# Optimization experiments

Hardware: AMD Instinct MI355X
Metric: run time of the kernel (lower is better)

Reference implementation:

```python
import jax, jax.numpy as jnp
import numpy as np

EPS_PD = 1e-6    # torch F.pairwise_distance eps (added to x - y before norm)
EPS_NORM = 1e-12  # torch F.normalize eps


def l2_normalize(x):
    n = jnp.sqrt(jnp.sum(x * x, axis=1, keepdims=True))
    return x / jnp.maximum(n, EPS_NORM)


def pairwise_l2(x, y):
    # Faithful to ||x_i - y_j + eps||_2 (torch pairwise_distance adds scalar eps
    # to every coordinate of the difference) but computed via Gram matrices
    D = x.shape[1]
    xx = jnp.sum(x * x, axis=1)            # [B]
    yy = jnp.sum(y * y, axis=1)            # [B]
    xy = x @ y.T                           # [B, B]
    sq = xx[:, None] + yy[None, :] - 2.0 * xy
    # cross terms from the +eps shift: 2*eps*sum(x_i - y_j) + D*eps^2
    sq = sq + 2.0 * EPS_PD * (jnp.sum(x, axis=1)[:, None] - jnp.sum(y, axis=1)[None, :])
    sq = sq + D * (EPS_PD * EPS_PD)
    return jnp.sqrt(jnp.maximum(sq, 0.0))


def setup_inputs() -> dict:
    key = jax.random.key(0)
    k1, k2 = jax.random.split(key)
    B, D = 4096, 512
    low_feature = jax.random.normal(k1, (B, D), dtype=jnp.float32)
    embed_feature = jax.random.normal(k2, (B, D), dtype=jnp.float32)
    id_numpy = jnp.arange(B, dtype=jnp.int64 if jax.config.read('jax_enable_x64') else jnp.int32).reshape(B, 1)
    return {"low_feature": low_feature, "embed_feature": embed_feature, "id_numpy": id_numpy}


def reference(low_feature, embed_feature, id_numpy):
    # ids are unique (arange), so the set()-dedup in the original is identity.
    B = low_feature.shape[0]
    K = B  # k_num == current_batch_size -> x_start = y_start = 0

    low_n = l2_normalize(low_feature)
    emb_n = l2_normalize(embed_feature)

    dist_low = pairwise_l2(low_n, low_n)      # [B, B]
    dist_embed = pairwise_l2(emb_n, emb_n)    # [B, B]

    dl1 = dist_low[: K - 1, : K - 2]
    dl2 = dist_low[: K - 1, 1 : K - 1]
    de1 = dist_embed[: K - 1, : K - 2]
    de2 = dist_embed[: K - 1, 1 : K - 1]

    coeff = jnp.sign(dl1 - dl2) - jnp.sign(de1 - de2)
    dist_embed_inverse = de2 - de1
    loss_structure = jnp.mean(coeff * dist_embed_inverse)
    return loss_structure
```

## Files before the change

### kernel.cpp

```cpp
#include <hip/hip_runtime.h>
#include <hip/hip_bf16.h>
#include <hip/hip_fp8.h>
#include <math.h>

#define BROWS 4096
#define DIM   512
#define YEMB_B 2097152
#define TSTRIDE 191
#define NT 22

typedef float f32x4 __attribute__((ext_vector_type(4)));

__global__ __launch_bounds__(256) void prep4_kernel(
    const float* __restrict__ low, const float* __restrict__ emb,
    unsigned char* __restrict__ Yq,
    float* __restrict__ s_l, float* __restrict__ r_l,
    float* __restrict__ s_e, float* __restrict__ r_e,
    float* __restrict__ out) {
  const int tid = threadIdx.x;
  const int lane = tid & 63, wid = tid >> 6;
  const int rid = blockIdx.x * 4 + wid;
  if (blockIdx.x == 0 && tid == 0) out[0] = 0.f;

  const bool is_low = (rid < BROWS);
  const int row = is_low ? rid : rid - BROWS;
  const float* x = (is_low ? low : emb) + (size_t)row * DIM;

  const float4 v0 = ((const float4*)x)[lane * 2];
  const float4 v1 = ((const float4*)x)[lane * 2 + 1];

  float ss = v0.x * v0.x + v0.y * v0.y + v0.z * v0.z + v0.w * v0.w +
             v1.x * v1.x + v1.y * v1.y + v1.z * v1.z + v1.w * v1.w;
#pragma unroll
  for (int o = 1; o < 64; o <<= 1) ss += __shfl_xor(ss, o, 64);
  const float inv = 1.0f / fmaxf(sqrtf(ss), 1e-12f);

  float y[8] = {v0.x * inv, v0.y * inv, v0.z * inv, v0.w * inv,
                v1.x * inv, v1.y * inv, v1.z * inv, v1.w * inv};

  union { unsigned char b[8]; unsigned long long u; } pk;
  float sv = 0.f, rv = 0.f;
#pragma unroll
  for (int i = 0; i < 8; ++i) {
    pk.b[i] = __hip_fp8_e4m3(y[i]).__x;
    sv += y[i] * y[i];
    rv += y[i];
  }
  ((unsigned long long*)(Yq + (size_t)rid * 512))[lane] = pk.u;

#pragma unroll
  for (int o = 1; o < 64; o <<= 1) {
    sv += __shfl_xor(sv, o, 64);
    rv += __shfl_xor(rv, o, 64);
  }
  if (lane == 0) {
    (is_low ? s_l : s_e)[row] = sv;
    (is_low ? r_l : r_e)[row] = rv;
  }
}

__global__ __launch_bounds__(256, 2) void fused_sym_kernel(
    const unsigned char* __restrict__ Yq,
    const float* __restrict__ s_l, const float* __restrict__ r_l,
    const float* __restrict__ s_e, const float* __restrict__ r_e,
    float* __restrict__ out) {
  __shared__ __align__(16) long lds_l[9728];
  __shared__ __align__(16) float aE[192];
  __shared__ __align__(16) float bE[120];
  __shared__ __align__(16) float cL[120];
  __shared__ float sred[4];

  const int b2 = blockIdx.x >> 1;
  const int half = blockIdx.x & 1;
  const int br = b2 / NT;
  const int bc = b2 % NT;

  const int tid = threadIdx.x;
  const int lane = tid & 63;
  const int wid = tid >> 6;
  const int wr = wid;
  const int quad = lane >> 4, cpos = lane & 15;
  const int r0 = br * TSTRIDE;
  const int cB = bc * TSTRIDE + half * 96;
  const int tcbase = half * 96;
  const float epst = (float)DIM * 1e-6f * 1e-6f;

  if (tid < 192) {
    const int gi = min(r0 + tid, BROWS - 1);
    aE[tid] = s_e[gi] + 2e-6f * r_e[gi] + epst;
  }
  if (tid < 116) {
    const int gj = min(cB + tid, BROWS - 1);
    const int gj1 = min(cB + tid + 1, BROWS - 1);
    bE[tid] = s_e[gj] - 2e-6f * r_e[gj];
    cL[tid] = (s_l[gj] - s_l[gj1]) - 2e-6f * (r_l[gj] - r_l[gj1]);
  }

  int goff[10];
#pragma unroll
  for (int s = 0; s < 10; ++s) {
    const int c = tid + 256 * s;
    const int rp = c >> 3, cc = c & 7;
    int seg, rpl;
    if (rp < 96)       { seg = 0; rpl = rp;       }
    else if (rp < 192) { seg = 1; rpl = rp - 96;  }
    else if (rp < 248) { seg = 2; rpl = rp - 192; }
    else               { seg = 3; rpl = rp - 248; }
    const int rloc = 2 * rpl + (cc >> 2);
    const int gch = (cc & 3) ^ (rpl & 3);
    int base;
    if (seg == 0)      base = min(r0 + rloc, BROWS - 1) * 512;
    else if (seg == 1) base = YEMB_B + min(r0 + rloc, BROWS - 1) * 512;
    else if (seg == 2) base = min(cB + rloc, BROWS - 1) * 512;
    else               base = YEMB_B + min(cB + rloc, BROWS - 1) * 512;
    goff[s] = base + (gch << 4);
  }

  auto STAGE = [&](int t, int b) {
    const int k0 = t * 64;
#pragma unroll
    for (int s = 0; s < 10; ++s) {
      if (s < 9 || tid < 128)
        __builtin_amdgcn_global_load_lds(
            (const __attribute__((address_space(1))) void*)(Yq + goff[s] + k0),
            (__attribute__((address_space(3))) void*)(
                ((char*)lds_l) + b * 38912 + (tid + 256 * s) * 16),
            16, 0, 0);
    }
  };

  const int RaH = (48 * wr + cpos) >> 1;
  const int s3a = RaH & 3;
  const int aoff = RaH * 128 + (cpos & 1) * 64 + (quad & 1) * 8;
  const int s3b = (cpos >> 1) & 3;
  const int boff = (cpos >> 1) * 128 + (cpos & 1) * 64 + (quad & 1) * 8;
  const int iaL = aoff >> 3;
  const int iaE = (12288 + aoff) >> 3;
  const int ibL = (24576 + boff) >> 3;
  const int ibE = (31744 + boff) >> 3;

  f32x4 accl[7][3], acce[7][3];
#pragma unroll
  for (int jb = 0; jb < 7; ++jb)
#pragma unroll
    for (int ib = 0; ib < 3; ++ib) {
      accl[jb][ib] = (f32x4)(0.f);
      acce[jb][ib] = (f32x4)(0.f);
    }

  STAGE(0, 0);

  for (int t = 0; t < 8; ++t) {
    if (t < 7) STAGE(t + 1, (t + 1) & 1);
    if (t == 7)       asm volatile("s_waitcnt vmcnt(0)" ::: "memory");
    else if (wid < 2) asm volatile("s_waitcnt vmcnt(10)" ::: "memory");
    else              asm volatile("s_waitcnt vmcnt(9)" ::: "memory");
    __builtin_amdgcn_s_barrier();
    __builtin_amdgcn_sched_barrier(0);

    const int bo = (t & 1) * 4864;
#pragma unroll
    for (int kk = 0; kk < 2; ++kk) {
      const int q = 2 * kk + (quad >> 1);
      const int qa2 = ((q ^ s3a) << 1);
      const int qb2 = ((q ^ s3b) << 1);
      {
        long a[7], b[3];
#pragma unroll
        for (int jb = 0; jb < 7; ++jb) a[jb] = lds_l[bo + ibL + qb2 + jb * 128];
#pragma unroll
        for (int ib = 0; ib < 3; ++ib) b[ib] = lds_l[bo + iaL + qa2 + ib * 128];
        __builtin_amdgcn_s_setprio(1);
#pragma unroll
        for (int jb = 0; jb < 7; ++jb)
#pragma unroll
          for (int ib = 0; ib < 3; ++ib)
            accl[jb][ib] = __builtin_amdgcn_mfma_f32_16x16x32_fp8_fp8(
                a[jb], b[ib], accl[jb][ib], 0, 0, 0);
        __builtin_amdgcn_s_setprio(0);
      }
      {
        long a[7], b[3];
#pragma unroll
        for (int jb = 0; jb < 7; ++jb) a[jb] = lds_l[bo + ibE + qb2 + jb * 128];
#pragma unroll
        for (int ib = 0; ib < 3; ++ib) b[ib] = lds_l[bo + iaE + qa2 + ib * 128];
        __builtin_amdgcn_s_setprio(1);
#pragma unroll
        for (int jb = 0; jb < 7; ++jb)
#pragma unroll
          for (int ib = 0; ib < 3; ++ib)
            acce[jb][ib] = __builtin_amdgcn_mfma_f32_16x16x32_fp8_fp8(
                a[jb], b[ib], acce[jb][ib], 0, 0, 0);
        __builtin_amdgcn_s_setprio(0);
      }
    }
    __builtin_amdgcn_sched_barrier(0);
    __builtin_amdgcn_s_barrier();
    __builtin_amdgcn_sched_barrier(0);
  }

  float sum = 0.f;

#pragma unroll
  for (int ib = 0; ib < 3; ++ib) {
    const int irow = 48 * wr + 16 * ib + cpos;
    const int gi = r0 + irow;
    const bool rowok = (irow <= TSTRIDE - 1) && (gi <= BROWS - 2);
    const float ai = aE[irow];

    float deJ[4], glJ[4];
    {
      const float4 bj = ((const float4*)bE)[quad];
#pragma unroll
      for (int r = 0; r < 4; ++r) {
        deJ[r] = sqrtf(fmaxf(ai + bj[r] - 2.f * acce[0][ib][r], 0.f));
        glJ[r] = accl[0][ib][r];
      }
    }

#pragma unroll
    for (int jb = 0; jb < 6; ++jb) {
      const float4 bn = ((const float4*)bE)[4 * (jb + 1) + quad];
      float deN[4], glN[4];
#pragma unroll
      for (int r = 0; r < 4; ++r) {
        deN[r] = sqrtf(fmaxf(ai + bn[r] - 2.f * acce[jb + 1][ib][r], 0.f));
        glN[r] = accl[jb + 1][ib][r];
      }
      const float deq = __shfl(deJ[0], (lane + 16) & 63, 64);
      const float dec = __shfl(deN[0], lane & 15, 64);
      const float glq = __shfl(glJ[0], (lane + 16) & 63, 64);
      const float glc = __shfl(glN[0], lane & 15, 64);
      const float de2r3 = (quad < 3) ? deq : dec;
      const float gl2r3 = (quad < 3) ? glq : glc;

      const float4 cl = ((const float4*)cL)[4 * jb + quad];
#pragma unroll
      for (int r = 0; r < 4; ++r) {
        const float de1 = deJ[r];
        const float de2 = (r < 3) ? deJ[r + 1] : de2r3;
        const float g2 = (r < 3) ? glJ[r + 1] : gl2r3;
        const float x = de2 - de1;
        const float Dl = cl[r] - 2.f * (glJ[r] - g2);
        const float tterm = fabsf(x) +
                            (Dl > 0.f ? x : (Dl < 0.f ? -x : 0.f));
        const int jcol = tcbase + 16 * jb + 4 * quad + r;
        const int gj = cB + 16 * jb + 4 * quad + r;
        if (rowok && jcol <= TSTRIDE - 1 && gj <= BROWS - 3) sum += tterm;
      }
#pragma unroll
      for (int r = 0; r < 4; ++r) { deJ[r] = deN[r]; glJ[r] = glN[r]; }
    }
  }

#pragma unroll
  for (int o = 32; o; o >>= 1) sum += __shfl_down(sum, o, 64);
  if (lane == 0) sred[wid] = sum;
  __syncthreads();
  if (tid == 0) {
    const float scale = 1.0f / ((float)(BROWS - 1) * (float)(BROWS - 2));
    float t = 0.f;
#pragma unroll
    for (int w = 0; w < 4; ++w) t += sred[w];
    atomicAdd(out, t * scale);
  }
}

extern "C" void kernel_launch(void* const* d_in, const int* in_sizes, int n_in,
                              void* d_out, int out_size, void* d_ws,
                              size_t ws_size, hipStream_t stream) {
  const float* low = (const float*)d_in[0];
  const float* emb = (const float*)d_in[1];
  float* out = (float*)d_out;

  unsigned char* Yq = (unsigned char*)d_ws;
  float* s_l = (float*)(Yq + 2 * (size_t)BROWS * DIM);
  float* r_l = s_l + BROWS;
  float* s_e = r_l + BROWS;
  float* r_e = s_e + BROWS;

  prep4_kernel<<<2 * BROWS / 4, 256, 0, stream>>>(low, emb, Yq, s_l, r_l, s_e, r_e, out);
  fused_sym_kernel<<<NT * NT * 2, 256, 0, stream>>>(Yq, s_l, r_l, s_e, r_e, out);
}
```

Baseline: 119.8 us.

## Exploit Gram matrix symmetry to compute only upper-triangular tiles

Launches only the upper-triangular tile pairs (br<=bc) and, for off-diagonal tiles, also evaluates the transposed contribution by taking differences along rows instead of columns. Cross-tile neighbors come from shuffles and a small LDS hand-off buffer. This roughly halves the MFMA and load work. The K loop also changes to 32-byte stages with a triple-buffered LDS pipeline and a new swizzle, and the unused seventh column block in the odd half is skipped. It adds extra epilogue shuffles and LDS traffic, and the boundary masking is tricky and could be wrong.

```diff
diff --git a/kernel.cpp b/kernel.cpp
--- a/kernel.cpp
+++ b/kernel.cpp
@@ -64,21 +64,24 @@
     const float* __restrict__ s_l, const float* __restrict__ r_l,
     const float* __restrict__ s_e, const float* __restrict__ r_e,
     float* __restrict__ out) {
-  __shared__ __align__(16) long lds_l[9728];
+  __shared__ __align__(16) long lds_l[7680];
   __shared__ __align__(16) float aE[192];
   __shared__ __align__(16) float bE[120];
   __shared__ __align__(16) float cL[120];
+  __shared__ __align__(16) float cLi[192];
+  __shared__ float hand[3][112][2];
   __shared__ float sred[4];
 
-  const int b2 = blockIdx.x >> 1;
   const int half = blockIdx.x & 1;
-  const int br = b2 / NT;
-  const int bc = b2 % NT;
+  int rem = blockIdx.x >> 1, br = 0;
+  while (rem >= NT - br) { rem -= NT - br; ++br; }
+  const int bc = br + rem;
+  const bool diag = (br == bc);
+  const bool hasv6 = (half == 0);
 
   const int tid = threadIdx.x;
   const int lane = tid & 63;
-  const int wid = tid >> 6;
-  const int wr = wid;
+  const int wr = tid >> 6;
   const int quad = lane >> 4, cpos = lane & 15;
   const int r0 = br * TSTRIDE;
   const int cB = bc * TSTRIDE + half * 96;
@@ -87,7 +90,9 @@
 
   if (tid < 192) {
     const int gi = min(r0 + tid, BROWS - 1);
+    const int gi1 = min(r0 + tid + 1, BROWS - 1);
     aE[tid] = s_e[gi] + 2e-6f * r_e[gi] + epst;
+    cLi[tid] = (s_l[gi] - s_l[gi1]) + 2e-6f * (r_l[gi] - r_l[gi1]);
   }
   if (tid < 116) {
     const int gj = min(cB + tid, BROWS - 1);
@@ -96,48 +101,50 @@
     cL[tid] = (s_l[gj] - s_l[gj1]) - 2e-6f * (r_l[gj] - r_l[gj1]);
   }
 
-  int goff[10];
-#pragma unroll
-  for (int s = 0; s < 10; ++s) {
+  int goff[5];
+#pragma unroll
+  for (int s = 0; s < 5; ++s) {
     const int c = tid + 256 * s;
-    const int rp = c >> 3, cc = c & 7;
-    int seg, rpl;
-    if (rp < 96)       { seg = 0; rpl = rp;       }
-    else if (rp < 192) { seg = 1; rpl = rp - 96;  }
-    else if (rp < 248) { seg = 2; rpl = rp - 192; }
-    else               { seg = 3; rpl = rp - 248; }
-    const int rloc = 2 * rpl + (cc >> 2);
-    const int gch = (cc & 3) ^ (rpl & 3);
-    int base;
-    if (seg == 0)      base = min(r0 + rloc, BROWS - 1) * 512;
-    else if (seg == 1) base = YEMB_B + min(r0 + rloc, BROWS - 1) * 512;
-    else if (seg == 2) base = min(cB + rloc, BROWS - 1) * 512;
-    else               base = YEMB_B + min(cB + rloc, BROWS - 1) * 512;
-    goff[s] = base + (gch << 4);
+    int seg, base;
+    if (c < 384)      { seg = 0; base = 0; }
+    else if (c < 768) { seg = 1; base = 384; }
+    else if (c < 992) { seg = 2; base = 768; }
+    else              { seg = 3; base = 992; }
+    const int within = c - base;
+    const int rpl = within >> 2, cc = within & 3;
+    const int rloc = 2 * rpl + ((cc >> 1) ^ ((rpl >> 1) & 1));
+    const int g = (cc & 1) ^ (rpl & 1);
+    int rowb;
+    if (seg == 0)      rowb = min(r0 + rloc, BROWS - 1) * 512;
+    else if (seg == 1) rowb = YEMB_B + min(r0 + rloc, BROWS - 1) * 512;
+    else if (seg == 2) rowb = min(cB + rloc, BROWS - 1) * 512;
+    else               rowb = YEMB_B + min(cB + rloc, BROWS - 1) * 512;
+    goff[s] = rowb + g * 16;
   }
 
   auto STAGE = [&](int t, int b) {
-    const int k0 = t * 64;
-#pragma unroll
-    for (int s = 0; s < 10; ++s) {
-      if (s < 9 || tid < 128)
+    const int k0 = t * 32;
+#pragma unroll
+    for (int s = 0; s < 5; ++s) {
+      if (s < 4 || tid < 192)
         __builtin_amdgcn_global_load_lds(
             (const __attribute__((address_space(1))) void*)(Yq + goff[s] + k0),
             (__attribute__((address_space(3))) void*)(
-                ((char*)lds_l) + b * 38912 + (tid + 256 * s) * 16),
+                ((char*)lds_l) + b * 20480 + (tid + 256 * s) * 16),
             16, 0, 0);
     }
   };
 
   const int RaH = (48 * wr + cpos) >> 1;
-  const int s3a = RaH & 3;
-  const int aoff = RaH * 128 + (cpos & 1) * 64 + (quad & 1) * 8;
-  const int s3b = (cpos >> 1) & 3;
-  const int boff = (cpos >> 1) * 128 + (cpos & 1) * 64 + (quad & 1) * 8;
-  const int iaL = aoff >> 3;
-  const int iaE = (12288 + aoff) >> 3;
-  const int ibL = (24576 + boff) >> 3;
-  const int ibE = (31744 + boff) >> 3;
+  const int offA = RaH * 64 + (((cpos & 1) ^ ((RaH >> 1) & 1)) << 5) +
+                   (((quad >> 1) ^ (RaH & 1)) << 4) + (quad & 1) * 8;
+  const int RbH = cpos >> 1;
+  const int offB = RbH * 64 + (((cpos & 1) ^ ((RbH >> 1) & 1)) << 5) +
+                   (((quad >> 1) ^ (RbH & 1)) << 4) + (quad & 1) * 8;
+  const int iaL = offA >> 3;
+  const int iaE = (6144 + offA) >> 3;
+  const int ibL = (12288 + offB) >> 3;
+  const int ibE = (15872 + offB) >> 3;
 
   f32x4 accl[7][3], acce[7][3];
 #pragma unroll
@@ -149,56 +156,84 @@
     }
 
   STAGE(0, 0);
-
-  for (int t = 0; t < 8; ++t) {
-    if (t < 7) STAGE(t + 1, (t + 1) & 1);
-    if (t == 7)       asm volatile("s_waitcnt vmcnt(0)" ::: "memory");
-    else if (wid < 2) asm volatile("s_waitcnt vmcnt(10)" ::: "memory");
-    else              asm volatile("s_waitcnt vmcnt(9)" ::: "memory");
+  STAGE(1, 1);
+
+  int bcur = 0;
+  for (int t = 0; t < 16; ++t) {
+    if (t < 14) STAGE(t + 2, (t + 2) % 3);
+    if (t < 14) {
+      if (wr < 3) asm volatile("s_waitcnt vmcnt(10)" ::: "memory");
+      else        asm volatile("s_waitcnt vmcnt(8)" ::: "memory");
+    } else if (t == 14) {
+      if (wr < 3) asm volatile("s_waitcnt vmcnt(5)" ::: "memory");
+      else        asm volatile("s_waitcnt vmcnt(4)" ::: "memory");
+    } else {
+      asm volatile("s_waitcnt vmcnt(0)" ::: "memory");
+    }
     __builtin_amdgcn_s_barrier();
     __builtin_amdgcn_sched_barrier(0);
 
-    const int bo = (t & 1) * 4864;
-#pragma unroll
-    for (int kk = 0; kk < 2; ++kk) {
-      const int q = 2 * kk + (quad >> 1);
-      const int qa2 = ((q ^ s3a) << 1);
-      const int qb2 = ((q ^ s3b) << 1);
-      {
-        long a[7], b[3];
-#pragma unroll
-        for (int jb = 0; jb < 7; ++jb) a[jb] = lds_l[bo + ibL + qb2 + jb * 128];
-#pragma unroll
-        for (int ib = 0; ib < 3; ++ib) b[ib] = lds_l[bo + iaL + qa2 + ib * 128];
-        __builtin_amdgcn_s_setprio(1);
-#pragma unroll
-        for (int jb = 0; jb < 7; ++jb)
+    const int bo = bcur * 2560;
+    {
+      long p[7], q[3];
+#pragma unroll
+      for (int jb = 0; jb < 7; ++jb) p[jb] = lds_l[bo + ibL + jb * 64];
+#pragma unroll
+      for (int ib = 0; ib < 3; ++ib) q[ib] = lds_l[bo + iaL + ib * 64];
+      __builtin_amdgcn_s_setprio(1);
+#pragma unroll
+      for (int jb = 0; jb < 7; ++jb)
+        if (jb < 6 || hasv6)
 #pragma unroll
           for (int ib = 0; ib < 3; ++ib)
             accl[jb][ib] = __builtin_amdgcn_mfma_f32_16x16x32_fp8_fp8(
-                a[jb], b[ib], accl[jb][ib], 0, 0, 0);
-        __builtin_amdgcn_s_setprio(0);
-      }
-      {
-        long a[7], b[3];
-#pragma unroll
-        for (int jb = 0; jb < 7; ++jb) a[jb] = lds_l[bo + ibE + qb2 + jb * 128];
-#pragma unroll
-        for (int ib = 0; ib < 3; ++ib) b[ib] = lds_l[bo + iaE + qa2 + ib * 128];
-        __builtin_amdgcn_s_setprio(1);
-#pragma unroll
-        for (int jb = 0; jb < 7; ++jb)
+                p[jb], q[ib], accl[jb][ib], 0, 0, 0);
+      __builtin_amdgcn_s_setprio(0);
+    }
+    {
+      long p[7], q[3];
+#pragma unroll
+      for (int jb = 0; jb < 7; ++jb) p[jb] = lds_l[bo + ibE + jb * 64];
+#pragma unroll
+      for (int ib = 0; ib < 3; ++ib) q[ib] = lds_l[bo + iaE + ib * 64];
+      __builtin_amdgcn_s_setprio(1);
+#pragma unroll
+      for (int jb = 0; jb < 7; ++jb)
+        if (jb < 6 || hasv6)
 #pragma unroll
           for (int ib = 0; ib < 3; ++ib)
             acce[jb][ib] = __builtin_amdgcn_mfma_f32_16x16x32_fp8_fp8(
-                a[jb], b[ib], acce[jb][ib], 0, 0, 0);
-        __builtin_amdgcn_s_setprio(0);
-      }
+                p[jb], q[ib], acce[jb][ib], 0, 0, 0);
+      __builtin_amdgcn_s_setprio(0);
     }
     __builtin_amdgcn_sched_barrier(0);
     __builtin_amdgcn_s_barrier();
     __builtin_amdgcn_sched_barrier(0);
-  }
+    bcur = (bcur == 2) ? 0 : bcur + 1;
+  }
+
+#pragma unroll
+  for (int ib = 0; ib < 3; ++ib) {
+    const float ai = aE[48 * wr + 16 * ib + cpos];
+#pragma unroll
+    for (int jb = 0; jb < 7; ++jb) {
+      const float4 be4 = ((const float4*)bE)[4 * jb + quad];
+#pragma unroll
+      for (int r = 0; r < 4; ++r)
+        acce[jb][ib][r] = sqrtf(fmaxf(ai + be4[r] - 2.f * acce[jb][ib][r], 0.f));
+    }
+  }
+
+  if (wr >= 1 && cpos == 0) {
+#pragma unroll
+    for (int jb = 0; jb < 7; ++jb)
+#pragma unroll
+      for (int r = 0; r < 4; ++r) {
+        hand[wr - 1][16 * jb + 4 * quad + r][0] = acce[jb][0][r];
+        hand[wr - 1][16 * jb + 4 * quad + r][1] = accl[jb][0][r];
+      }
+  }
+  __syncthreads();
 
   float sum = 0.f;
 
@@ -207,56 +242,68 @@
     const int irow = 48 * wr + 16 * ib + cpos;
     const int gi = r0 + irow;
     const bool rowok = (irow <= TSTRIDE - 1) && (gi <= BROWS - 2);
-    const float ai = aE[irow];
-
-    float deJ[4], glJ[4];
-    {
-      const float4 bj = ((const float4*)bE)[quad];
-#pragma unroll
-      for (int r = 0; r < 4; ++r) {
-        deJ[r] = sqrtf(fmaxf(ai + bj[r] - 2.f * acce[0][ib][r], 0.f));
-        glJ[r] = accl[0][ib][r];
-      }
-    }
-
 #pragma unroll
     for (int jb = 0; jb < 6; ++jb) {
-      const float4 bn = ((const float4*)bE)[4 * (jb + 1) + quad];
-      float deN[4], glN[4];
-#pragma unroll
-      for (int r = 0; r < 4; ++r) {
-        deN[r] = sqrtf(fmaxf(ai + bn[r] - 2.f * acce[jb + 1][ib][r], 0.f));
-        glN[r] = accl[jb + 1][ib][r];
-      }
-      const float deq = __shfl(deJ[0], (lane + 16) & 63, 64);
-      const float dec = __shfl(deN[0], lane & 15, 64);
-      const float glq = __shfl(glJ[0], (lane + 16) & 63, 64);
-      const float glc = __shfl(glN[0], lane & 15, 64);
+      const float deq = __shfl(acce[jb][ib][0], (lane + 16) & 63, 64);
+      const float glq = __shfl(accl[jb][ib][0], (lane + 16) & 63, 64);
+      const float dec = __shfl(acce[jb + 1][ib][0], lane & 15, 64);
+      const float glc = __shfl(accl[jb + 1][ib][0], lane & 15, 64);
       const float de2r3 = (quad < 3) ? deq : dec;
       const float gl2r3 = (quad < 3) ? glq : glc;
-
-      const float4 cl = ((const float4*)cL)[4 * jb + quad];
+      const float4 cl4 = ((const float4*)cL)[4 * jb + quad];
 #pragma unroll
       for (int r = 0; r < 4; ++r) {
-        const float de1 = deJ[r];
-        const float de2 = (r < 3) ? deJ[r + 1] : de2r3;
-        const float g2 = (r < 3) ? glJ[r + 1] : gl2r3;
+        const float de1 = acce[jb][ib][r], g1 = accl[jb][ib][r];
+        const float de2 = (r < 3) ? acce[jb][ib][r + 1] : de2r3;
+        const float g2 = (r < 3) ? accl[jb][ib][r + 1] : gl2r3;
         const float x = de2 - de1;
-        const float Dl = cl[r] - 2.f * (glJ[r] - g2);
-        const float tterm = fabsf(x) +
-                            (Dl > 0.f ? x : (Dl < 0.f ? -x : 0.f));
-        const int jcol = tcbase + 16 * jb + 4 * quad + r;
-        const int gj = cB + 16 * jb + 4 * quad + r;
-        if (rowok && jcol <= TSTRIDE - 1 && gj <= BROWS - 3) sum += tterm;
+        const float Dl = cl4[r] - 2.f * (g1 - g2);
+        const float term = fabsf(x) + (Dl > 0.f ? x : (Dl < 0.f ? -x : 0.f));
+        const int c1 = 16 * jb + 4 * quad + r;
+        if (rowok && tcbase + c1 <= TSTRIDE - 1 && cB + c1 <= BROWS - 3)
+          sum += term;
       }
-#pragma unroll
-      for (int r = 0; r < 4; ++r) { deJ[r] = deN[r]; glJ[r] = glN[r]; }
+    }
+  }
+
+  if (!diag) {
+    const int hw = (wr < 3) ? wr : 2;
+#pragma unroll
+    for (int ib = 0; ib < 3; ++ib) {
+      const int irow = 48 * wr + 16 * ib + cpos;
+      const int gi = r0 + irow;
+      const bool bok = (irow <= TSTRIDE - 1) && (gi <= BROWS - 3);
+      const float cli = cLi[irow];
+#pragma unroll
+      for (int jb = 0; jb < 6; ++jb) {
+#pragma unroll
+        for (int r = 0; r < 4; ++r) {
+          const float de1 = acce[jb][ib][r], g1 = accl[jb][ib][r];
+          const int srcn = (lane & 48) | ((cpos + 1) & 15);
+          float de2 = __shfl(de1, srcn, 64);
+          float g2 = __shfl(g1, srcn, 64);
+          if (ib < 2) {
+            const float dei = __shfl(acce[jb][ib + 1][r], lane & 48, 64);
+            const float gli = __shfl(accl[jb][ib + 1][r], lane & 48, 64);
+            if (cpos == 15) { de2 = dei; g2 = gli; }
+          } else {
+            const int a = 16 * jb + 4 * quad + r;
+            if (cpos == 15) { de2 = hand[hw][a][0]; g2 = hand[hw][a][1]; }
+          }
+          const float x = de2 - de1;
+          const float Dl = cli - 2.f * (g1 - g2);
+          const float term = fabsf(x) + (Dl > 0.f ? x : (Dl < 0.f ? -x : 0.f));
+          const int a = 16 * jb + 4 * quad + r;
+          if (bok && tcbase + a <= TSTRIDE - 1 && cB + a <= BROWS - 2)
+            sum += term;
+        }
+      }
     }
   }
 
 #pragma unroll
   for (int o = 32; o; o >>= 1) sum += __shfl_down(sum, o, 64);
-  if (lane == 0) sred[wid] = sum;
+  if (lane == 0) sred[wr] = sum;
   __syncthreads();
   if (tid == 0) {
     const float scale = 1.0f / ((float)(BROWS - 1) * (float)(BROWS - 2));
@@ -281,5 +328,5 @@
   float* r_e = s_e + BROWS;
 
   prep4_kernel<<<2 * BROWS / 4, 256, 0, stream>>>(low, emb, Yq, s_l, r_l, s_e, r_e, out);
-  fused_sym_kernel<<<NT * NT * 2, 256, 0, stream>>>(Yq, s_l, r_l, s_e, r_e, out);
+  fused_sym_kernel<<<NT * (NT + 1), 256, 0, stream>>>(Yq, s_l, r_l, s_e, r_e, out);
 }
```

Result: slower. 138.3 us (+15.4%).
